# Performance work log

Hardware: AMD Instinct MI355X
Metric: run time of the kernel (lower is better)

Reference implementation:

```python
import jax, jax.numpy as jnp
import numpy as np

B, CIN, HIN, WIN = 64, 64, 128, 128
COUT, K = 64, 3
S, P, OP = 2, 1, 1   # stride, padding, output_padding
MULT = 0.5


def setup_inputs() -> dict:
    key = jax.random.key(0)
    k1, k2, k3 = jax.random.split(key, 3)
    x = jax.random.normal(k1, (B, CIN, HIN, WIN), dtype=jnp.float32)
    # ConvTranspose2d weight layout: [Cin, Cout, kH, kW]
    weight = jax.random.normal(k2, (CIN, COUT, K, K), dtype=jnp.float32) * 0.05
    bias = jax.random.normal(k3, (COUT,), dtype=jnp.float32) * 0.05
    return {"x": x, "weight": weight, "bias": bias}


def reference(x, weight, bias):
    # Fused conv_transpose2d -> *multiplier -> global mean over (H,W),
    # computed algebraically without materializing the [B,Cout,Hout,Wout] map.
    Hout = (HIN - 1) * S - 2 * P + (K - 1) + OP + 1   # = 256
    Wout = (WIN - 1) * S - 2 * P + (K - 1) + OP + 1   # = 256

    # Validity masks: output position oh = ih*S - P + kh must lie in [0, Hout)
    oh = jnp.arange(HIN)[:, None] * S - P + jnp.arange(K)[None, :]  # [Hin, K]
    ow = jnp.arange(WIN)[:, None] * S - P + jnp.arange(K)[None, :]
    Vh = ((oh >= 0) & (oh < Hout)).astype(x.dtype)  # [Hin, K]
    Vw = ((ow >= 0) & (ow < Wout)).astype(x.dtype)

    # Masked spatial sums of x per kernel offset: [B, Cin, K, K]
    sx = jnp.einsum('bchw,hk,wl->bckl', x, Vh, Vw)
    # Contract with weight over (Cin, kH, kW): [B, Cout]
    acc = jnp.einsum('bckl,cokl->bo', sx, weight)

    out = (acc / (Hout * Wout) + bias[None, :]) * MULT
    return out[:, :, None, None]  # [B, Cout, 1, 1]
```

## Files before the change

### kernel.cpp

```cpp
#include <hip/hip_runtime.h>


#define N_PLANES 4096
#define CIN 64
#define COUT 64
#define PLANE_F4 4096

__global__ __launch_bounds__(256) void plane_reduce(const float* __restrict__ x,
                                                    float4* __restrict__ sx4) {
    const int plane = blockIdx.x;
    const float4* xp = reinterpret_cast<const float4*>(x) + (size_t)plane * PLANE_F4;
    const int t = threadIdx.x;

    float T = 0.f, R0 = 0.f, C0 = 0.f, X00 = 0.f;
#pragma unroll
    for (int i = 0; i < 16; ++i) {
        const int f = i * 256 + t;
        const float4 v = xp[f];
        const float s4 = v.x + v.y + v.z + v.w;
        T += s4;
        if (f < 32) R0 += s4;
        if ((f & 31) == 0) C0 += v.x;
        if (f == 0) X00 = v.x;
    }

#pragma unroll
    for (int off = 32; off > 0; off >>= 1) {
        T  += __shfl_down(T,  off);
        R0 += __shfl_down(R0, off);
        C0 += __shfl_down(C0, off);
    }

    __shared__ float sT[4], sR[4], sC[4];
    const int wave = t >> 6;
    if ((t & 63) == 0) { sT[wave] = T; sR[wave] = R0; sC[wave] = C0; }
    __syncthreads();
    if (t == 0) {
        sx4[plane] = make_float4(sT[0] + sT[1] + sT[2] + sT[3],
                                 sR[0] + sR[1] + sR[2] + sR[3],
                                 sC[0] + sC[1] + sC[2] + sC[3],
                                 X00);
    }
}

__global__ __launch_bounds__(256) void weight_prep(const float* __restrict__ w,
                                                   float4* __restrict__ w4) {
    const int idx = blockIdx.x * 256 + threadIdx.x;
    if (idx >= CIN * COUT) return;
    const float* wp = w + (size_t)idx * 9;
    const float a0 = wp[0], a1 = wp[1], a2 = wp[2],
                a3 = wp[3], a4 = wp[4], a5 = wp[5],
                a6 = wp[6], a7 = wp[7], a8 = wp[8];
    const float wsum = a0 + a1 + a2 + a3 + a4 + a5 + a6 + a7 + a8;
    const float wrow = a0 + a1 + a2;
    const float wcol = a0 + a3 + a6;
    w4[idx] = make_float4(wsum, wrow, wcol, a0);
}

__global__ __launch_bounds__(64) void finalize(const float4* __restrict__ sx4,
                                               const float4* __restrict__ w4,
                                               const float* __restrict__ bias,
                                               float* __restrict__ out) {
    const int b = blockIdx.x;
    const int o = threadIdx.x;

    __shared__ float4 s[CIN];
    s[o] = sx4[b * CIN + o];
    __syncthreads();

    float acc = 0.f;
#pragma unroll 8
    for (int c = 0; c < CIN; ++c) {
        const float4 sv = s[c];
        const float4 wv = w4[c * COUT + o];
        acc += sv.x * wv.x - sv.y * wv.y - sv.z * wv.z + sv.w * wv.w;
    }
    out[b * COUT + o] = (acc * (1.0f / 65536.0f) + bias[o]) * 0.5f;
}

extern "C" void kernel_launch(void* const* d_in, const int* in_sizes, int n_in,
                              void* d_out, int out_size, void* d_ws, size_t ws_size,
                              hipStream_t stream) {
    const float* x    = (const float*)d_in[0];
    const float* w    = (const float*)d_in[1];
    const float* bias = (const float*)d_in[2];
    float* out = (float*)d_out;

    float4* sx4 = (float4*)d_ws;
    float4* w4  = sx4 + N_PLANES;

    plane_reduce<<<N_PLANES, 256, 0, stream>>>(x, sx4);
    weight_prep<<<(CIN * COUT + 255) / 256, 256, 0, stream>>>(w, w4);
    finalize<<<64, 64, 0, stream>>>(sx4, w4, bias, out);
}
```

Baseline: 50.55 us.

## Fuse reduce, weight prep and finalize into one kernel with last-block completion

Merges the three launches into a single kernel. Producer blocks each reduce two planes, extra blocks precompute the weight sums, and the last block to bump an atomic counter runs the final contraction for all batches. This removes two kernel launches and the gaps between them. The cost is a memset launch, a serial tail in which one 256-thread block computes the whole 64x64 output, and halving the number of producer blocks.

After: 146.1 us. 2.89x slower.

```diff
diff --git a/kernel.cpp b/kernel.cpp
--- a/kernel.cpp
+++ b/kernel.cpp
@@ -1,81 +1,109 @@
 #include <hip/hip_runtime.h>
 
 
-#define N_PLANES 4096
 #define CIN 64
 #define COUT 64
+#define N_PLANES 4096
 #define PLANE_F4 4096
+#define PROD_BLOCKS 2048
+#define W_BLOCKS 16
+#define TOTAL_BLOCKS (PROD_BLOCKS + W_BLOCKS)
 
-__global__ __launch_bounds__(256) void plane_reduce(const float* __restrict__ x,
-                                                    float4* __restrict__ sx4) {
-    const int plane = blockIdx.x;
-    const float4* xp = reinterpret_cast<const float4*>(x) + (size_t)plane * PLANE_F4;
+__global__ __launch_bounds__(256) void fused_all(const float* __restrict__ x,
+                                                 const float* __restrict__ w,
+                                                 const float* __restrict__ bias,
+                                                 float* __restrict__ out,
+                                                 float* __restrict__ sx,
+                                                 float* __restrict__ wm,
+                                                 unsigned* __restrict__ counter) {
     const int t = threadIdx.x;
+    const int blk = blockIdx.x;
+    __shared__ float sT[2][4], sR[2][4], sC[2][4];
+    __shared__ unsigned s_old;
 
-    float T = 0.f, R0 = 0.f, C0 = 0.f, X00 = 0.f;
+    if (blk < PROD_BLOCKS) {
+        float X00[2];
 #pragma unroll
-    for (int i = 0; i < 16; ++i) {
-        const int f = i * 256 + t;
-        const float4 v = xp[f];
-        const float s4 = v.x + v.y + v.z + v.w;
-        T += s4;
-        if (f < 32) R0 += s4;
-        if ((f & 31) == 0) C0 += v.x;
-        if (f == 0) X00 = v.x;
+        for (int p = 0; p < 2; ++p) {
+            const int plane = blk * 2 + p;
+            const float4* xp = reinterpret_cast<const float4*>(x) + (size_t)plane * PLANE_F4;
+            float T = 0.f, R0 = 0.f, C0 = 0.f, X = 0.f;
+#pragma unroll
+            for (int i = 0; i < 16; ++i) {
+                const int f = i * 256 + t;
+                const float4 v = xp[f];
+                const float s4 = (v.x + v.y) + (v.z + v.w);
+                T += s4;
+                if (f < 32) R0 += s4;
+                if ((t & 31) == 0) C0 += v.x;
+                if (f == 0) X = v.x;
+            }
+#pragma unroll
+            for (int off = 32; off > 0; off >>= 1) {
+                T  += __shfl_down(T, off);
+                R0 += __shfl_down(R0, off);
+                C0 += __shfl_down(C0, off);
+            }
+            const int wave = t >> 6;
+            if ((t & 63) == 0) { sT[p][wave] = T; sR[p][wave] = R0; sC[p][wave] = C0; }
+            X00[p] = X;
+        }
+        __syncthreads();
+        if (t == 0) {
+#pragma unroll
+            for (int p = 0; p < 2; ++p) {
+                const int plane = blk * 2 + p;
+                const float Tt = (sT[p][0] + sT[p][1]) + (sT[p][2] + sT[p][3]);
+                const float Rr = (sR[p][0] + sR[p][1]) + (sR[p][2] + sR[p][3]);
+                const float Cc = (sC[p][0] + sC[p][1]) + (sC[p][2] + sC[p][3]);
+                __hip_atomic_store(&sx[plane * 4 + 0], Tt,     __ATOMIC_RELAXED, __HIP_MEMORY_SCOPE_AGENT);
+                __hip_atomic_store(&sx[plane * 4 + 1], Rr,     __ATOMIC_RELAXED, __HIP_MEMORY_SCOPE_AGENT);
+                __hip_atomic_store(&sx[plane * 4 + 2], Cc,     __ATOMIC_RELAXED, __HIP_MEMORY_SCOPE_AGENT);
+                __hip_atomic_store(&sx[plane * 4 + 3], X00[p], __ATOMIC_RELAXED, __HIP_MEMORY_SCOPE_AGENT);
+            }
+        }
+    } else {
+        const int idx = (blk - PROD_BLOCKS) * 256 + t;
+        const float* wp = w + (size_t)idx * 9;
+        const float a0 = wp[0], a1 = wp[1], a2 = wp[2],
+                    a3 = wp[3], a4 = wp[4], a5 = wp[5],
+                    a6 = wp[6], a7 = wp[7], a8 = wp[8];
+        const float wsum = ((a0 + a1) + (a2 + a3)) + ((a4 + a5) + (a6 + a7)) + a8;
+        const float wrow = a0 + a1 + a2;
+        const float wcol = a0 + a3 + a6;
+        __hip_atomic_store(&wm[idx * 4 + 0], wsum, __ATOMIC_RELAXED, __HIP_MEMORY_SCOPE_AGENT);
+        __hip_atomic_store(&wm[idx * 4 + 1], wrow, __ATOMIC_RELAXED, __HIP_MEMORY_SCOPE_AGENT);
+        __hip_atomic_store(&wm[idx * 4 + 2], wcol, __ATOMIC_RELAXED, __HIP_MEMORY_SCOPE_AGENT);
+        __hip_atomic_store(&wm[idx * 4 + 3], a0,   __ATOMIC_RELAXED, __HIP_MEMORY_SCOPE_AGENT);
     }
 
-#pragma unroll
-    for (int off = 32; off > 0; off >>= 1) {
-        T  += __shfl_down(T,  off);
-        R0 += __shfl_down(R0, off);
-        C0 += __shfl_down(C0, off);
-    }
-
-    __shared__ float sT[4], sR[4], sC[4];
-    const int wave = t >> 6;
-    if ((t & 63) == 0) { sT[wave] = T; sR[wave] = R0; sC[wave] = C0; }
     __syncthreads();
     if (t == 0) {
-        sx4[plane] = make_float4(sT[0] + sT[1] + sT[2] + sT[3],
-                                 sR[0] + sR[1] + sR[2] + sR[3],
-                                 sC[0] + sC[1] + sC[2] + sC[3],
-                                 X00);
+        s_old = __hip_atomic_fetch_add(counter, 1u, __ATOMIC_ACQ_REL, __HIP_MEMORY_SCOPE_AGENT);
     }
-}
+    __syncthreads();
+    if (s_old != TOTAL_BLOCKS - 1) return;
 
-__global__ __launch_bounds__(256) void weight_prep(const float* __restrict__ w,
-                                                   float4* __restrict__ w4) {
-    const int idx = blockIdx.x * 256 + threadIdx.x;
-    if (idx >= CIN * COUT) return;
-    const float* wp = w + (size_t)idx * 9;
-    const float a0 = wp[0], a1 = wp[1], a2 = wp[2],
-                a3 = wp[3], a4 = wp[4], a5 = wp[5],
-                a6 = wp[6], a7 = wp[7], a8 = wp[8];
-    const float wsum = a0 + a1 + a2 + a3 + a4 + a5 + a6 + a7 + a8;
-    const float wrow = a0 + a1 + a2;
-    const float wcol = a0 + a3 + a6;
-    w4[idx] = make_float4(wsum, wrow, wcol, a0);
-}
-
-__global__ __launch_bounds__(64) void finalize(const float4* __restrict__ sx4,
-                                               const float4* __restrict__ w4,
-                                               const float* __restrict__ bias,
-                                               float* __restrict__ out) {
-    const int b = blockIdx.x;
-    const int o = threadIdx.x;
-
-    __shared__ float4 s[CIN];
-    s[o] = sx4[b * CIN + o];
-    __syncthreads();
-
-    float acc = 0.f;
-#pragma unroll 8
+    __threadfence();
+    const int o  = t & 63;
+    const int bg = t >> 6;
+    float acc[16];
+#pragma unroll
+    for (int k = 0; k < 16; ++k) acc[k] = 0.f;
+    const float4* sq = reinterpret_cast<const float4*>(sx);
+    const float4* wq = reinterpret_cast<const float4*>(wm);
     for (int c = 0; c < CIN; ++c) {
-        const float4 sv = s[c];
-        const float4 wv = w4[c * COUT + o];
-        acc += sv.x * wv.x - sv.y * wv.y - sv.z * wv.z + sv.w * wv.w;
+        const float4 wv = wq[c * COUT + o];
+#pragma unroll
+        for (int k = 0; k < 16; ++k) {
+            const float4 q = sq[(bg * 16 + k) * CIN + c];
+            acc[k] += q.x * wv.x - q.y * wv.y - q.z * wv.z + q.w * wv.w;
+        }
     }
-    out[b * COUT + o] = (acc * (1.0f / 65536.0f) + bias[o]) * 0.5f;
+    const float bo = bias[o];
+#pragma unroll
+    for (int k = 0; k < 16; ++k)
+        out[(bg * 16 + k) * COUT + o] = (acc[k] * (1.0f / 65536.0f) + bo) * 0.5f;
 }
 
 extern "C" void kernel_launch(void* const* d_in, const int* in_sizes, int n_in,
@@ -86,10 +114,10 @@
     const float* bias = (const float*)d_in[2];
     float* out = (float*)d_out;
 
-    float4* sx4 = (float4*)d_ws;
-    float4* w4  = sx4 + N_PLANES;
+    float* sx = (float*)d_ws;
+    float* wm = sx + N_PLANES * 4;
+    unsigned* counter = (unsigned*)((char*)d_ws + 131072);
 
-    plane_reduce<<<N_PLANES, 256, 0, stream>>>(x, sx4);
-    weight_prep<<<(CIN * COUT + 255) / 256, 256, 0, stream>>>(w, w4);
-    finalize<<<64, 64, 0, stream>>>(sx4, w4, bias, out);
+    hipMemsetAsync(counter, 0, sizeof(unsigned), stream);
+    fused_all<<<TOTAL_BLOCKS, 256, 0, stream>>>(x, w, bias, out, sx, wm, counter);
 }
```
